# Performance work log

Measured on AMD Instinct MI355X. Metric: run time of the kernel, lower is better.

## Reference

```python
import jax, jax.numpy as jnp
import numpy as np

D_MAX = 0.5      # max_dist init kwarg
EPS_W = 1e-8     # weight for far edges
EPS_L = 1e-5     # diagonal jitter on projected Laplacian


def setup_inputs() -> dict:
    key = jax.random.key(0)
    k1, k2, k3, k4, k5 = jax.random.split(key, 5)
    V, d_feat, E, K = 8192, 128, 262144, 512
    # scale so squared distances straddle D_MAX (both branches taken)
    inputs = jax.random.normal(k1, (V, d_feat), dtype=jnp.float32) * 0.05
    src = jax.random.randint(k2, (E,), 0, V)
    off = jax.random.randint(k3, (E,), 1, V)  # avoid self-loops
    dst = (src + off) % V
    edge_index = jnp.stack([src, dst]).astype(jnp.int32)
    A = jax.random.normal(k4, (K, K), dtype=jnp.float32)
    targets = A @ A.T / K + jnp.eye(K, dtype=jnp.float32)  # SPD covariance
    pmat = jax.random.normal(k5, (K, V), dtype=jnp.float32) / np.float32(np.sqrt(V))
    return {"inputs": inputs, "targets": targets, "edge_index": edge_index, "pmat": pmat}


def reference(inputs, targets, edge_index, pmat):
    V = inputs.shape[0]
    K = pmat.shape[0]
    src, dst = edge_index[0], edge_index[1]
    # vectorized per-edge squared distance + thresholded weight
    d = jnp.sum((inputs[src] - inputs[dst]) ** 2, axis=-1)            # [E]
    w = jnp.where(d <= D_MAX, jnp.exp(-d), jnp.float32(EPS_W))        # [E]
    # W = I on diag, w on (i,j) and (j,i) for edges, 0 elsewhere
    W = jnp.eye(V, dtype=inputs.dtype).at[src, dst].set(w).at[dst, src].set(w)
    deg = W.sum(axis=1)                                               # [V]
    idx = jnp.arange(V)
    L = (-W).at[idx, idx].add(deg)                                    # Laplacian D - W
    L_adj = (pmat @ L) @ pmat.T + EPS_L * jnp.eye(K, dtype=inputs.dtype)
    # log det(inv(L_adj)) = -logdet(L_adj); trace(L_adj @ S0) = sum(L_adj * S0^T)
    logdet_Ladj = jnp.linalg.slogdet(L_adj)[1]
    logdet_S0 = jnp.linalg.slogdet(targets)[1]
    tr = jnp.sum(L_adj * targets.T)
    return -logdet_Ladj - logdet_S0 - jnp.float32(K) + tr
```

## Files before the change

### kernel.cpp

```cpp
#include <hip/hip_runtime.h>
#include <math.h>

#define V_N 8192
#define D_F 128
#define E_N 262144
#define K_N 512
#define DMAXF 0.5f
#define EPSW 1e-8f
#define EPSL 1e-5f
#define MAX_SE 16384
#define NZ_SYRK 24

#define NB_TR 4096
#define NB_ED (E_N / 16)
#define NB_CP 256

__global__ __launch_bounds__(256) void k_pre(const float* __restrict__ P, float* __restrict__ PT,
                                             const float* __restrict__ X, const int* __restrict__ ei,
                                             int* __restrict__ cnt, int* __restrict__ si,
                                             int* __restrict__ sj, float* __restrict__ sw,
                                             unsigned* __restrict__ htab,
                                             const float* __restrict__ T, float* __restrict__ Lw1) {
  __shared__ float tile[32][33];
  int b = blockIdx.x;
  if (b < NB_TR) {
    int v0 = (b & 255) * 32, k0 = (b >> 8) * 32;
    int tx = threadIdx.x & 31, ty = threadIdx.x >> 5;
#pragma unroll
    for (int i = 0; i < 4; ++i)
      tile[ty + i * 8][tx] = P[(size_t)(k0 + ty + i * 8) * V_N + v0 + tx];
    __syncthreads();
#pragma unroll
    for (int i = 0; i < 4; ++i)
      PT[(size_t)(v0 + ty + i * 8) * K_N + k0 + tx] = tile[tx][ty + i * 8];
  } else if (b < NB_TR + NB_ED) {
    int t = (b - NB_TR) * 256 + threadIdx.x;
    int e = t >> 4, lane = t & 15;
    int i = ei[e], j = ei[E_N + e];
    const float4* xi = (const float4*)(X + (size_t)i * D_F);
    const float4* xj = (const float4*)(X + (size_t)j * D_F);
    float4 a0 = xi[lane * 2], a1 = xi[lane * 2 + 1];
    float4 b0 = xj[lane * 2], b1 = xj[lane * 2 + 1];
    float d = 0.f, dx;
    dx = a0.x - b0.x; d += dx * dx;
    dx = a0.y - b0.y; d += dx * dx;
    dx = a0.z - b0.z; d += dx * dx;
    dx = a0.w - b0.w; d += dx * dx;
    dx = a1.x - b1.x; d += dx * dx;
    dx = a1.y - b1.y; d += dx * dx;
    dx = a1.z - b1.z; d += dx * dx;
    dx = a1.w - b1.w; d += dx * dx;
    d += __shfl_xor(d, 1);
    d += __shfl_xor(d, 2);
    d += __shfl_xor(d, 4);
    d += __shfl_xor(d, 8);
    if (lane == 0 && d <= DMAXF) {
      float w = expf(-d);
      unsigned a = (unsigned)min(i, j), bb = (unsigned)max(i, j);
      unsigned key = a * 8192u + bb;
      unsigned h = (key * 2654435761u) >> 16;
      bool isnew = false;
      for (int probe = 0; probe < 65536; ++probe) {
        unsigned slot = (h + (unsigned)probe) & 65535u;
        unsigned prev = atomicCAS(&htab[slot], 0u, key);
        if (prev == 0u) { isnew = true; break; }
        if (prev == key) break;
      }
      if (isnew) {
        int p = atomicAdd(cnt, 1);
        if (p < MAX_SE) { si[p] = i; sj[p] = j; sw[p] = w; }
      }
    }
  } else {
    int idx = (b - NB_TR - NB_ED) * 256 + threadIdx.x;
    ((float4*)Lw1)[idx] = ((const float4*)T)[idx];
  }
}

__global__ __launch_bounds__(256) void k_syrk(const int* __restrict__ cnt, const int* __restrict__ si,
                                              const int* __restrict__ sj, const float* __restrict__ sw,
                                              const float* __restrict__ PT, float* __restrict__ La,
                                              const float* __restrict__ T, float* __restrict__ tr) {
  int p = blockIdx.x, bj = 0;
  while (p >= 8 - bj) { p -= 8 - bj; ++bj; }
  int bi = bj + p;
  int r0g = bi * 64, c0g = bj * 64;
  int m = min(*cnt, MAX_SE);
  int chunk = (m + NZ_SYRK - 1) / NZ_SYRK;
  int e0 = blockIdx.y * chunk;
  int e1 = min(m, e0 + chunk);

  __shared__ float As[16][68];
  __shared__ float Bs[16][68];
  int tid = threadIdx.x;
  int le = tid >> 4, f = tid & 15;
  int r0 = (tid >> 4) * 4, c0 = (tid & 15) * 4;
  float acc[4][4];
#pragma unroll
  for (int i = 0; i < 4; ++i)
#pragma unroll
    for (int j = 0; j < 4; ++j) acc[i][j] = 0.f;

  float w_ = 0.f;
  float4 ai = make_float4(0.f, 0.f, 0.f, 0.f), aj = ai, ci = ai, cj = ai;
  {
    int e = e0 + le;
    if (e < e1) {
      int i = si[e], j = sj[e];
      w_ = sw[e];
      const float* pi = &PT[(size_t)i * K_N];
      const float* pj = &PT[(size_t)j * K_N];
      ai = *(const float4*)(pi + r0g + f * 4);
      aj = *(const float4*)(pj + r0g + f * 4);
      if (bi != bj) {
        ci = *(const float4*)(pi + c0g + f * 4);
        cj = *(const float4*)(pj + c0g + f * 4);
      }
    }
  }

  for (int es = e0; es < e1; es += 16) {
    float sq = sqrtf(w_);
    float4 qa, qb;
    qa.x = sq * (ai.x - aj.x); qa.y = sq * (ai.y - aj.y);
    qa.z = sq * (ai.z - aj.z); qa.w = sq * (ai.w - aj.w);
    if (bi != bj) {
      qb.x = sq * (ci.x - cj.x); qb.y = sq * (ci.y - cj.y);
      qb.z = sq * (ci.z - cj.z); qb.w = sq * (ci.w - cj.w);
    } else {
      qb = qa;
    }
    __syncthreads();
    *(float4*)&As[le][f * 4] = qa;
    *(float4*)&Bs[le][f * 4] = qb;
    __syncthreads();

    {
      int e = es + 16 + le;
      w_ = 0.f;
      if (e < e1) {
        int i = si[e], j = sj[e];
        w_ = sw[e];
        const float* pi = &PT[(size_t)i * K_N];
        const float* pj = &PT[(size_t)j * K_N];
        ai = *(const float4*)(pi + r0g + f * 4);
        aj = *(const float4*)(pj + r0g + f * 4);
        if (bi != bj) {
          ci = *(const float4*)(pi + c0g + f * 4);
          cj = *(const float4*)(pj + c0g + f * 4);
        }
      }
    }

#pragma unroll
    for (int k = 0; k < 16; ++k) {
      float4 av = *(const float4*)&As[k][r0];
      float4 bv = *(const float4*)&Bs[k][c0];
      acc[0][0] += av.x * bv.x; acc[0][1] += av.x * bv.y; acc[0][2] += av.x * bv.z; acc[0][3] += av.x * bv.w;
      acc[1][0] += av.y * bv.x; acc[1][1] += av.y * bv.y; acc[1][2] += av.y * bv.z; acc[1][3] += av.y * bv.w;
      acc[2][0] += av.z * bv.x; acc[2][1] += av.z * bv.y; acc[2][2] += av.z * bv.z; acc[2][3] += av.z * bv.w;
      acc[3][0] += av.w * bv.x; acc[3][1] += av.w * bv.y; acc[3][2] += av.w * bv.z; acc[3][3] += av.w * bv.w;
    }
  }

  bool addeps = (blockIdx.y == 0) && (bi == bj);
  float tdot = 0.f;
#pragma unroll
  for (int i = 0; i < 4; ++i)
#pragma unroll
    for (int j = 0; j < 4; ++j) {
      float v = acc[i][j];
      int rg = r0g + r0 + i, cg = c0g + c0 + j;
      if (addeps && rg == cg) v += EPSL;
      atomicAdd(&La[(size_t)rg * K_N + cg], v);
      float sc = (bi != bj) ? 2.f : (rg == cg ? 1.f : (rg > cg ? 2.f : 0.f));
      if (sc != 0.f) tdot += sc * v * T[(size_t)rg * K_N + cg];
    }
  tdot += __shfl_down(tdot, 32); tdot += __shfl_down(tdot, 16); tdot += __shfl_down(tdot, 8);
  tdot += __shfl_down(tdot, 4);  tdot += __shfl_down(tdot, 2);  tdot += __shfl_down(tdot, 1);
  if ((tid & 63) == 0) atomicAdd(tr, tdot);
}

__device__ __forceinline__ void factor32(float (*sm)[65], int o, int tid, float& logacc) {
  if (tid < 64) {
    int r = tid & 31;
    float a[32];
#pragma unroll
    for (int c = 0; c < 32; ++c) a[c] = sm[o + r][o + c];
    float ls = 0.f;
#pragma unroll
    for (int c = 0; c < 32; ++c) {
      float dc = __shfl(a[c], c);
      ls += logf(dc);
      float s_ = sqrtf(dc);
      a[c] = a[c] / s_;
#pragma unroll
      for (int k = c + 1; k < 32; ++k)
        a[k] -= a[c] * __shfl(a[c], k);
    }
    if (tid < 32) {
#pragma unroll
      for (int c = 0; c < 32; ++c) sm[o + r][o + c] = a[c];
    }
    if (tid == 0) logacc += ls;
  }
}

__global__ __launch_bounds__(512) void k_panel(float* La, float* Lw1, float* __restrict__ ld, int s) {
  float* A = (blockIdx.x == 0) ? La : Lw1;
  const int j0 = s * 64;
  int tid = threadIdx.x;
  __shared__ float sm[64][65];
  __shared__ float smT[64][68];
  __shared__ float rinv[64];
  float logacc = 0.f;

  for (int i = tid; i < 4096; i += 512) {
    int r = i >> 6, c = i & 63;
    sm[r][c] = A[(size_t)(j0 + r) * K_N + j0 + c];
  }
  __syncthreads();

  factor32(sm, 0, tid, logacc);
  __syncthreads();

  if (tid < 32) {
    int r = 32 + tid;
    float x[32];
#pragma unroll
    for (int c = 0; c < 32; ++c) x[c] = sm[r][c];
#pragma unroll
    for (int c = 0; c < 32; ++c) {
      x[c] = x[c] / sm[c][c];
#pragma unroll
      for (int k = c + 1; k < 32; ++k)
        x[k] -= x[c] * sm[k][c];
    }
#pragma unroll
    for (int c = 0; c < 32; ++c) sm[r][c] = x[c];
  }
  __syncthreads();

  for (int i = tid; i < 1024; i += 512) {
    int r = 32 + (i >> 5), c = 32 + (i & 31);
    float accv = 0.f;
#pragma unroll
    for (int k = 0; k < 32; ++k) accv += sm[r][k] * sm[c][k];
    sm[r][c] -= accv;
  }
  __syncthreads();

  factor32(sm, 32, tid, logacc);
  __syncthreads();

  for (int i = tid; i < 4096; i += 512) {
    int r = i >> 6, c = i & 63;
    smT[c][r] = sm[r][c];
  }
  if (tid < 64) rinv[tid] = 1.0f / sm[tid][tid];
  __syncthreads();

  int rrow = j0 + 64 + tid;
  if (rrow < K_N) {
    float x[64];
#pragma unroll
    for (int q = 0; q < 16; ++q) {
      float4 f = *(const float4*)&A[(size_t)rrow * K_N + j0 + 4 * q];
      x[4 * q] = f.x; x[4 * q + 1] = f.y; x[4 * q + 2] = f.z; x[4 * q + 3] = f.w;
    }
#pragma unroll
    for (int c = 0; c < 64; ++c) {
      x[c] *= rinv[c];
#pragma unroll
      for (int k = c + 1; k < 64; ++k)
        x[k] -= x[c] * smT[c][k];
    }
#pragma unroll
    for (int q = 0; q < 16; ++q) {
      float4 f;
      f.x = x[4 * q]; f.y = x[4 * q + 1]; f.z = x[4 * q + 2]; f.w = x[4 * q + 3];
      *(float4*)&A[(size_t)rrow * K_N + j0 + 4 * q] = f;
    }
  }

  for (int i = tid; i < 4096; i += 512) {
    int r = i >> 6, c = i & 63;
    A[(size_t)(j0 + r) * K_N + j0 + c] = sm[r][c];
  }
  if (tid == 0) ld[blockIdx.x * 8 + s] = logacc;
}

__global__ __launch_bounds__(256) void k_update(float* La, float* Lw1, int s) {
  float* A = (blockIdx.y == 0) ? La : Lw1;
  int nt = 7 - s;
  int p = blockIdx.x;
  int bj = 0;
  while (p >= nt - bj) { p -= nt - bj; ++bj; }
  int bi = bj + p;
  int r0g = (s + 1 + bi) * 64, c0g = (s + 1 + bj) * 64, k0g = s * 64;

  __shared__ float As[64][68];
  __shared__ float Bs[64][68];
  int tid = threadIdx.x;
  for (int i = tid; i < 1024; i += 256) {
    int r = i >> 4, kq = (i & 15) << 2;
    float4 f = *(const float4*)&A[(size_t)(r0g + r) * K_N + k0g + kq];
    As[kq + 0][r] = f.x; As[kq + 1][r] = f.y; As[kq + 2][r] = f.z; As[kq + 3][r] = f.w;
    float4 g = *(const float4*)&A[(size_t)(c0g + r) * K_N + k0g + kq];
    Bs[kq + 0][r] = g.x; Bs[kq + 1][r] = g.y; Bs[kq + 2][r] = g.z; Bs[kq + 3][r] = g.w;
  }
  __syncthreads();

  int r0 = (tid >> 4) * 4, c0 = (tid & 15) * 4;
  float acc[4][4];
#pragma unroll
  for (int i = 0; i < 4; ++i)
#pragma unroll
    for (int j = 0; j < 4; ++j) acc[i][j] = 0.f;
#pragma unroll 4
  for (int k = 0; k < 64; ++k) {
    float4 av = *(const float4*)&As[k][r0];
    float4 bv = *(const float4*)&Bs[k][c0];
    acc[0][0] += av.x * bv.x; acc[0][1] += av.x * bv.y; acc[0][2] += av.x * bv.z; acc[0][3] += av.x * bv.w;
    acc[1][0] += av.y * bv.x; acc[1][1] += av.y * bv.y; acc[1][2] += av.y * bv.z; acc[1][3] += av.y * bv.w;
    acc[2][0] += av.z * bv.x; acc[2][1] += av.z * bv.y; acc[2][2] += av.z * bv.z; acc[2][3] += av.z * bv.w;
    acc[3][0] += av.w * bv.x; acc[3][1] += av.w * bv.y; acc[3][2] += av.w * bv.z; acc[3][3] += av.w * bv.w;
  }
#pragma unroll
  for (int i = 0; i < 4; ++i) {
    float* cp = &A[(size_t)(r0g + r0 + i) * K_N + c0g + c0];
#pragma unroll
    for (int j = 0; j < 4; ++j) cp[j] = cp[j] - acc[i][j];
  }
}

__global__ void k_combine(const float* __restrict__ ld, const float* __restrict__ tr, float* __restrict__ out) {
  float l0 = 0.f, l1 = 0.f;
#pragma unroll
  for (int s = 0; s < 8; ++s) { l0 += ld[s]; l1 += ld[8 + s]; }
  out[0] = -l0 - l1 - (float)K_N + tr[0];
}

extern "C" void kernel_launch(void* const* d_in, const int* in_sizes, int n_in,
                              void* d_out, int out_size, void* d_ws, size_t ws_size,
                              hipStream_t stream) {
  const float* X  = (const float*)d_in[0];
  const float* T  = (const float*)d_in[1];
  const int*   ei = (const int*)d_in[2];
  const float* P  = (const float*)d_in[3];
  float* out = (float*)d_out;
  char* ws = (char*)d_ws;

  int*      cnt  = (int*)(ws + 0);
  float*    tr   = (float*)(ws + 16);
  float*    ld   = (float*)(ws + 32);
  unsigned* htab = (unsigned*)(ws + 4096);
  float*    La   = (float*)(ws + 266240);
  float*    Lw1  = (float*)(ws + 1314816);
  int*      si   = (int*)(ws + 2363392);
  int*      sj   = (int*)(ws + 2428928);
  float*    sw   = (float*)(ws + 2494464);
  float*    PT   = (float*)(ws + 2560000);

  hipMemsetAsync(ws, 0, 1314816, stream);

  k_pre<<<NB_TR + NB_ED + NB_CP, 256, 0, stream>>>(P, PT, X, ei, cnt, si, sj, sw, htab, T, Lw1);
  k_syrk<<<dim3(36, NZ_SYRK), 256, 0, stream>>>(cnt, si, sj, sw, PT, La, T, tr);

  for (int s = 0; s < 8; ++s) {
    k_panel<<<2, 512, 0, stream>>>(La, Lw1, ld, s);
    int nt = 7 - s;
    if (nt > 0) k_update<<<dim3(nt * (nt + 1) / 2, 2), 256, 0, stream>>>(La, Lw1, s);
  }
  k_combine<<<1, 1, 0, stream>>>(ld, tr, out);
}
```

Measured before the change: 553.0 us.

## Fuse blocked Cholesky into one persistent kernel with grid barriers; split pre-kernel

Replaces the 8-step loop of panel and update launches with a single persistent kernel of 16 blocks, 8 per matrix. The blocks sync through global atomic barriers and do a look-ahead, where the diagonal tile is updated into shared memory and factored as one 64-wide block instead of two 32-wide halves. The pre-kernel is split into a transpose/copy kernel that now uses 64x64 tiles with float4 access, and a separate edge kernel that uses 8 lanes per edge instead of 16. The aim is to cut about 15 launch gaps from the serial factorization. The cost is that it relies on all blocks being co-resident for the spin barrier, and the fixed small grid limits parallelism in the update phase.

```diff
diff --git a/kernel.cpp b/kernel.cpp
--- a/kernel.cpp
+++ b/kernel.cpp
@@ -10,70 +10,76 @@
 #define EPSL 1e-5f
 #define MAX_SE 16384
 #define NZ_SYRK 24
-
-#define NB_TR 4096
-#define NB_ED (E_N / 16)
-#define NB_CP 256
-
-__global__ __launch_bounds__(256) void k_pre(const float* __restrict__ P, float* __restrict__ PT,
-                                             const float* __restrict__ X, const int* __restrict__ ei,
-                                             int* __restrict__ cnt, int* __restrict__ si,
-                                             int* __restrict__ sj, float* __restrict__ sw,
-                                             unsigned* __restrict__ htab,
-                                             const float* __restrict__ T, float* __restrict__ Lw1) {
-  __shared__ float tile[32][33];
-  int b = blockIdx.x;
-  if (b < NB_TR) {
-    int v0 = (b & 255) * 32, k0 = (b >> 8) * 32;
-    int tx = threadIdx.x & 31, ty = threadIdx.x >> 5;
-#pragma unroll
-    for (int i = 0; i < 4; ++i)
-      tile[ty + i * 8][tx] = P[(size_t)(k0 + ty + i * 8) * V_N + v0 + tx];
+#define LDS68 68
+
+__global__ __launch_bounds__(256) void k_tr(const float* __restrict__ P, float* __restrict__ PT,
+                                            const float* __restrict__ T, float* __restrict__ Lw1) {
+  int b = blockIdx.x, tid = threadIdx.x;
+  if (b < 1024) {
+    __shared__ float tl[64][65];
+    int v0 = (b & 127) * 64, k0 = (b >> 7) * 64;
+    int c4 = tid & 15, rq = tid >> 4;
+#pragma unroll
+    for (int rr = 0; rr < 4; ++rr) {
+      int r = rq + 16 * rr;
+      float4 f = *(const float4*)&P[(size_t)(k0 + r) * V_N + v0 + c4 * 4];
+      tl[r][c4 * 4 + 0] = f.x; tl[r][c4 * 4 + 1] = f.y;
+      tl[r][c4 * 4 + 2] = f.z; tl[r][c4 * 4 + 3] = f.w;
+    }
     __syncthreads();
 #pragma unroll
-    for (int i = 0; i < 4; ++i)
-      PT[(size_t)(v0 + ty + i * 8) * K_N + k0 + tx] = tile[tx][ty + i * 8];
-  } else if (b < NB_TR + NB_ED) {
-    int t = (b - NB_TR) * 256 + threadIdx.x;
-    int e = t >> 4, lane = t & 15;
-    int i = ei[e], j = ei[E_N + e];
-    const float4* xi = (const float4*)(X + (size_t)i * D_F);
-    const float4* xj = (const float4*)(X + (size_t)j * D_F);
-    float4 a0 = xi[lane * 2], a1 = xi[lane * 2 + 1];
-    float4 b0 = xj[lane * 2], b1 = xj[lane * 2 + 1];
-    float d = 0.f, dx;
-    dx = a0.x - b0.x; d += dx * dx;
-    dx = a0.y - b0.y; d += dx * dx;
-    dx = a0.z - b0.z; d += dx * dx;
-    dx = a0.w - b0.w; d += dx * dx;
-    dx = a1.x - b1.x; d += dx * dx;
-    dx = a1.y - b1.y; d += dx * dx;
-    dx = a1.z - b1.z; d += dx * dx;
-    dx = a1.w - b1.w; d += dx * dx;
-    d += __shfl_xor(d, 1);
-    d += __shfl_xor(d, 2);
-    d += __shfl_xor(d, 4);
-    d += __shfl_xor(d, 8);
-    if (lane == 0 && d <= DMAXF) {
-      float w = expf(-d);
-      unsigned a = (unsigned)min(i, j), bb = (unsigned)max(i, j);
-      unsigned key = a * 8192u + bb;
-      unsigned h = (key * 2654435761u) >> 16;
-      bool isnew = false;
-      for (int probe = 0; probe < 65536; ++probe) {
-        unsigned slot = (h + (unsigned)probe) & 65535u;
-        unsigned prev = atomicCAS(&htab[slot], 0u, key);
-        if (prev == 0u) { isnew = true; break; }
-        if (prev == key) break;
-      }
-      if (isnew) {
-        int p = atomicAdd(cnt, 1);
-        if (p < MAX_SE) { si[p] = i; sj[p] = j; sw[p] = w; }
-      }
+    for (int rr = 0; rr < 4; ++rr) {
+      int r = rq + 16 * rr;
+      float4 f;
+      f.x = tl[c4 * 4 + 0][r]; f.y = tl[c4 * 4 + 1][r];
+      f.z = tl[c4 * 4 + 2][r]; f.w = tl[c4 * 4 + 3][r];
+      *(float4*)&PT[(size_t)(v0 + r) * K_N + k0 + c4 * 4] = f;
     }
   } else {
-    int idx = (b - NB_TR - NB_ED) * 256 + threadIdx.x;
+    int idx = (b - 1024) * 256 + tid;
     ((float4*)Lw1)[idx] = ((const float4*)T)[idx];
+  }
+}
+
+__global__ __launch_bounds__(256) void k_edge(const float* __restrict__ X, const int* __restrict__ ei,
+                                              int* __restrict__ cnt, int* __restrict__ si,
+                                              int* __restrict__ sj, float* __restrict__ sw,
+                                              unsigned* __restrict__ htab) {
+  int t = blockIdx.x * 256 + threadIdx.x;
+  int e = t >> 3, lane = t & 7;
+  int i = ei[e], j = ei[E_N + e];
+  const float4* xi = (const float4*)(X + (size_t)i * D_F);
+  const float4* xj = (const float4*)(X + (size_t)j * D_F);
+  float4 A0 = xi[lane * 4 + 0], A1 = xi[lane * 4 + 1], A2 = xi[lane * 4 + 2], A3 = xi[lane * 4 + 3];
+  float4 B0 = xj[lane * 4 + 0], B1 = xj[lane * 4 + 1], B2 = xj[lane * 4 + 2], B3 = xj[lane * 4 + 3];
+  float d = 0.f, dx;
+  dx = A0.x - B0.x; d += dx * dx; dx = A0.y - B0.y; d += dx * dx;
+  dx = A0.z - B0.z; d += dx * dx; dx = A0.w - B0.w; d += dx * dx;
+  dx = A1.x - B1.x; d += dx * dx; dx = A1.y - B1.y; d += dx * dx;
+  dx = A1.z - B1.z; d += dx * dx; dx = A1.w - B1.w; d += dx * dx;
+  dx = A2.x - B2.x; d += dx * dx; dx = A2.y - B2.y; d += dx * dx;
+  dx = A2.z - B2.z; d += dx * dx; dx = A2.w - B2.w; d += dx * dx;
+  dx = A3.x - B3.x; d += dx * dx; dx = A3.y - B3.y; d += dx * dx;
+  dx = A3.z - B3.z; d += dx * dx; dx = A3.w - B3.w; d += dx * dx;
+  d += __shfl_xor(d, 1);
+  d += __shfl_xor(d, 2);
+  d += __shfl_xor(d, 4);
+  if (lane == 0 && d <= DMAXF) {
+    float w = expf(-d);
+    unsigned a = (unsigned)min(i, j), bb = (unsigned)max(i, j);
+    unsigned key = a * 8192u + bb;
+    unsigned h = (key * 2654435761u) >> 16;
+    bool isnew = false;
+    for (int probe = 0; probe < 65536; ++probe) {
+      unsigned slot = (h + (unsigned)probe) & 65535u;
+      unsigned prev = atomicCAS(&htab[slot], 0u, key);
+      if (prev == 0u) { isnew = true; break; }
+      if (prev == key) break;
+    }
+    if (isnew) {
+      int p = atomicAdd(cnt, 1);
+      if (p < MAX_SE) { si[p] = i; sj[p] = j; sw[p] = w; }
+    }
   }
 }
 
@@ -181,156 +187,180 @@
   if ((tid & 63) == 0) atomicAdd(tr, tdot);
 }
 
-__device__ __forceinline__ void factor32(float (*sm)[65], int o, int tid, float& logacc) {
-  if (tid < 64) {
-    int r = tid & 31;
-    float a[32];
-#pragma unroll
-    for (int c = 0; c < 32; ++c) a[c] = sm[o + r][o + c];
-    float ls = 0.f;
-#pragma unroll
-    for (int c = 0; c < 32; ++c) {
-      float dc = __shfl(a[c], c);
-      ls += logf(dc);
-      float s_ = sqrtf(dc);
-      a[c] = a[c] / s_;
-#pragma unroll
-      for (int k = c + 1; k < 32; ++k)
-        a[k] -= a[c] * __shfl(a[c], k);
-    }
-    if (tid < 32) {
-#pragma unroll
-      for (int c = 0; c < 32; ++c) sm[o + r][o + c] = a[c];
-    }
-    if (tid == 0) logacc += ls;
-  }
-}
-
-__global__ __launch_bounds__(512) void k_panel(float* La, float* Lw1, float* __restrict__ ld, int s) {
-  float* A = (blockIdx.x == 0) ? La : Lw1;
-  const int j0 = s * 64;
-  int tid = threadIdx.x;
-  __shared__ float sm[64][65];
-  __shared__ float smT[64][68];
-  __shared__ float rinv[64];
-  float logacc = 0.f;
-
-  for (int i = tid; i < 4096; i += 512) {
-    int r = i >> 6, c = i & 63;
-    sm[r][c] = A[(size_t)(j0 + r) * K_N + j0 + c];
-  }
+__device__ __forceinline__ void gbar(unsigned* c_, unsigned& ep) {
+  ep += 8;
   __syncthreads();
-
-  factor32(sm, 0, tid, logacc);
+  __threadfence();
+  if (threadIdx.x == 0) {
+    __hip_atomic_fetch_add(c_, 1u, __ATOMIC_RELEASE, __HIP_MEMORY_SCOPE_AGENT);
+    while (__hip_atomic_load(c_, __ATOMIC_ACQUIRE, __HIP_MEMORY_SCOPE_AGENT) < ep)
+      __builtin_amdgcn_s_sleep(2);
+  }
   __syncthreads();
-
-  if (tid < 32) {
-    int r = 32 + tid;
-    float x[32];
-#pragma unroll
-    for (int c = 0; c < 32; ++c) x[c] = sm[r][c];
-#pragma unroll
-    for (int c = 0; c < 32; ++c) {
-      x[c] = x[c] / sm[c][c];
-#pragma unroll
-      for (int k = c + 1; k < 32; ++k)
-        x[k] -= x[c] * sm[k][c];
-    }
-#pragma unroll
-    for (int c = 0; c < 32; ++c) sm[r][c] = x[c];
-  }
+  __threadfence();
+}
+
+__device__ __forceinline__ void factor64(float* A, int j0, const float* smFsrc,
+                                         float* ldout, int tid) {
+  if (tid >= 64) return;
+  int r = tid;
+  float a[64];
+  if (smFsrc) {
+#pragma unroll
+    for (int q = 0; q < 16; ++q) {
+      float4 f = *(const float4*)&smFsrc[r * LDS68 + q * 4];
+      a[q * 4 + 0] = f.x; a[q * 4 + 1] = f.y; a[q * 4 + 2] = f.z; a[q * 4 + 3] = f.w;
+    }
+  } else {
+#pragma unroll
+    for (int q = 0; q < 16; ++q) {
+      float4 f = *(const float4*)&A[(size_t)(j0 + r) * K_N + j0 + q * 4];
+      a[q * 4 + 0] = f.x; a[q * 4 + 1] = f.y; a[q * 4 + 2] = f.z; a[q * 4 + 3] = f.w;
+    }
+  }
+  float ls = 0.f;
+#pragma unroll
+  for (int c = 0; c < 64; ++c) {
+    float dc = __shfl(a[c], c);
+    ls += logf(dc);
+    float rs = rsqrtf(dc);
+    a[c] *= rs;
+#pragma unroll
+    for (int k = c + 1; k < 64; ++k)
+      a[k] -= a[c] * __shfl(a[c], k);
+  }
+#pragma unroll
+  for (int q = 0; q < 16; ++q) {
+    float4 f;
+    f.x = a[q * 4 + 0]; f.y = a[q * 4 + 1]; f.z = a[q * 4 + 2]; f.w = a[q * 4 + 3];
+    *(float4*)&A[(size_t)(j0 + r) * K_N + j0 + q * 4] = f;
+  }
+  if (r == 0) *ldout = ls;
+}
+
+__device__ __forceinline__ void upd_tile(float* A, int sbase, int q, int nt2, bool toSmF,
+                                         float* As_, float* Bs_, float* smF, int tid) {
+  int lbj = 0;
+  while (q >= nt2 - lbj) { q -= nt2 - lbj; ++lbj; }
+  int lbi = lbj + q;
+  int r0g = (sbase + lbi) * 64, c0g = (sbase + lbj) * 64, k0g = (sbase - 1) * 64;
   __syncthreads();
-
   for (int i = tid; i < 1024; i += 512) {
-    int r = 32 + (i >> 5), c = 32 + (i & 31);
-    float accv = 0.f;
-#pragma unroll
-    for (int k = 0; k < 32; ++k) accv += sm[r][k] * sm[c][k];
-    sm[r][c] -= accv;
-  }
-  __syncthreads();
-
-  factor32(sm, 32, tid, logacc);
-  __syncthreads();
-
-  for (int i = tid; i < 4096; i += 512) {
-    int r = i >> 6, c = i & 63;
-    smT[c][r] = sm[r][c];
-  }
-  if (tid < 64) rinv[tid] = 1.0f / sm[tid][tid];
-  __syncthreads();
-
-  int rrow = j0 + 64 + tid;
-  if (rrow < K_N) {
-    float x[64];
-#pragma unroll
-    for (int q = 0; q < 16; ++q) {
-      float4 f = *(const float4*)&A[(size_t)rrow * K_N + j0 + 4 * q];
-      x[4 * q] = f.x; x[4 * q + 1] = f.y; x[4 * q + 2] = f.z; x[4 * q + 3] = f.w;
-    }
-#pragma unroll
-    for (int c = 0; c < 64; ++c) {
-      x[c] *= rinv[c];
-#pragma unroll
-      for (int k = c + 1; k < 64; ++k)
-        x[k] -= x[c] * smT[c][k];
-    }
-#pragma unroll
-    for (int q = 0; q < 16; ++q) {
-      float4 f;
-      f.x = x[4 * q]; f.y = x[4 * q + 1]; f.z = x[4 * q + 2]; f.w = x[4 * q + 3];
-      *(float4*)&A[(size_t)rrow * K_N + j0 + 4 * q] = f;
-    }
-  }
-
-  for (int i = tid; i < 4096; i += 512) {
-    int r = i >> 6, c = i & 63;
-    A[(size_t)(j0 + r) * K_N + j0 + c] = sm[r][c];
-  }
-  if (tid == 0) ld[blockIdx.x * 8 + s] = logacc;
-}
-
-__global__ __launch_bounds__(256) void k_update(float* La, float* Lw1, int s) {
-  float* A = (blockIdx.y == 0) ? La : Lw1;
-  int nt = 7 - s;
-  int p = blockIdx.x;
-  int bj = 0;
-  while (p >= nt - bj) { p -= nt - bj; ++bj; }
-  int bi = bj + p;
-  int r0g = (s + 1 + bi) * 64, c0g = (s + 1 + bj) * 64, k0g = s * 64;
-
-  __shared__ float As[64][68];
-  __shared__ float Bs[64][68];
-  int tid = threadIdx.x;
-  for (int i = tid; i < 1024; i += 256) {
     int r = i >> 4, kq = (i & 15) << 2;
     float4 f = *(const float4*)&A[(size_t)(r0g + r) * K_N + k0g + kq];
-    As[kq + 0][r] = f.x; As[kq + 1][r] = f.y; As[kq + 2][r] = f.z; As[kq + 3][r] = f.w;
+    As_[(kq + 0) * LDS68 + r] = f.x; As_[(kq + 1) * LDS68 + r] = f.y;
+    As_[(kq + 2) * LDS68 + r] = f.z; As_[(kq + 3) * LDS68 + r] = f.w;
     float4 g = *(const float4*)&A[(size_t)(c0g + r) * K_N + k0g + kq];
-    Bs[kq + 0][r] = g.x; Bs[kq + 1][r] = g.y; Bs[kq + 2][r] = g.z; Bs[kq + 3][r] = g.w;
+    Bs_[(kq + 0) * LDS68 + r] = g.x; Bs_[(kq + 1) * LDS68 + r] = g.y;
+    Bs_[(kq + 2) * LDS68 + r] = g.z; Bs_[(kq + 3) * LDS68 + r] = g.w;
   }
   __syncthreads();
-
-  int r0 = (tid >> 4) * 4, c0 = (tid & 15) * 4;
-  float acc[4][4];
-#pragma unroll
-  for (int i = 0; i < 4; ++i)
+  int r0 = (tid >> 4) * 2, c0 = (tid & 15) * 4;
+  float acc[2][4];
+#pragma unroll
+  for (int i = 0; i < 2; ++i)
 #pragma unroll
     for (int j = 0; j < 4; ++j) acc[i][j] = 0.f;
-#pragma unroll 4
+#pragma unroll 8
   for (int k = 0; k < 64; ++k) {
-    float4 av = *(const float4*)&As[k][r0];
-    float4 bv = *(const float4*)&Bs[k][c0];
-    acc[0][0] += av.x * bv.x; acc[0][1] += av.x * bv.y; acc[0][2] += av.x * bv.z; acc[0][3] += av.x * bv.w;
-    acc[1][0] += av.y * bv.x; acc[1][1] += av.y * bv.y; acc[1][2] += av.y * bv.z; acc[1][3] += av.y * bv.w;
-    acc[2][0] += av.z * bv.x; acc[2][1] += av.z * bv.y; acc[2][2] += av.z * bv.z; acc[2][3] += av.z * bv.w;
-    acc[3][0] += av.w * bv.x; acc[3][1] += av.w * bv.y; acc[3][2] += av.w * bv.z; acc[3][3] += av.w * bv.w;
-  }
-#pragma unroll
-  for (int i = 0; i < 4; ++i) {
-    float* cp = &A[(size_t)(r0g + r0 + i) * K_N + c0g + c0];
-#pragma unroll
-    for (int j = 0; j < 4; ++j) cp[j] = cp[j] - acc[i][j];
+    float a0 = As_[k * LDS68 + r0], a1 = As_[k * LDS68 + r0 + 1];
+    float4 bv = *(const float4*)&Bs_[k * LDS68 + c0];
+    acc[0][0] += a0 * bv.x; acc[0][1] += a0 * bv.y; acc[0][2] += a0 * bv.z; acc[0][3] += a0 * bv.w;
+    acc[1][0] += a1 * bv.x; acc[1][1] += a1 * bv.y; acc[1][2] += a1 * bv.z; acc[1][3] += a1 * bv.w;
+  }
+  if (toSmF) {
+#pragma unroll
+    for (int i = 0; i < 2; ++i) {
+      const float* cp = &A[(size_t)(r0g + r0 + i) * K_N + c0g + c0];
+      float4 co = *(const float4*)cp;
+      smF[(r0 + i) * LDS68 + c0 + 0] = co.x - acc[i][0];
+      smF[(r0 + i) * LDS68 + c0 + 1] = co.y - acc[i][1];
+      smF[(r0 + i) * LDS68 + c0 + 2] = co.z - acc[i][2];
+      smF[(r0 + i) * LDS68 + c0 + 3] = co.w - acc[i][3];
+    }
+  } else {
+#pragma unroll
+    for (int i = 0; i < 2; ++i) {
+      float* cp = &A[(size_t)(r0g + r0 + i) * K_N + c0g + c0];
+      cp[0] -= acc[i][0]; cp[1] -= acc[i][1]; cp[2] -= acc[i][2]; cp[3] -= acc[i][3];
+    }
+  }
+}
+
+__global__ __launch_bounds__(512, 1) void k_chol2(float* La, float* Lw1, float* __restrict__ ld,
+                                                  unsigned* __restrict__ ctr) {
+  int mat = blockIdx.x >> 3;
+  int b = blockIdx.x & 7;
+  float* A = mat ? Lw1 : La;
+  unsigned* myctr = ctr + mat * 16;
+  int tid = threadIdx.x;
+  __shared__ float sh[3 * 64 * LDS68 + 64];
+  float* As_ = sh;
+  float* Bs_ = sh + 64 * LDS68;
+  float* smF = sh + 2 * 64 * LDS68;
+  float* rin = sh + 3 * 64 * LDS68;
+  unsigned ep = 0;
+  __threadfence();
+
+  for (int s = 0; s < 8; ++s) {
+    const int j0 = s * 64;
+    int rel = (b - s) & 7;
+    if (s == 0) {
+      if (b == 0) factor64(A, 0, nullptr, &ld[mat * 8], tid);
+    } else {
+      int nt2 = 8 - s;
+      int cntT = nt2 * (nt2 + 1) / 2;
+      if (rel == 0) {
+        upd_tile(A, s, 0, nt2, true, As_, Bs_, smF, tid);
+        __syncthreads();
+        factor64(A, j0, smF, &ld[mat * 8 + s], tid);
+      } else {
+        for (int q = rel; q < cntT; q += 7)
+          upd_tile(A, s, q, nt2, false, As_, Bs_, smF, tid);
+      }
+    }
+    gbar(myctr, ep);
+
+    if (b < 7 - s) {
+      __syncthreads();
+      for (int idx = tid; idx < 4096; idx += 512) {
+        int k = idx >> 6, c = idx & 63;
+        As_[c * LDS68 + k] = A[(size_t)(j0 + k) * K_N + j0 + c];
+      }
+      __syncthreads();
+      if (tid < 64) rin[tid] = 1.0f / As_[tid * LDS68 + tid];
+      __syncthreads();
+      if (tid < 64) {
+        int row = (s + 1 + b) * 64 + tid;
+        float x[64];
+#pragma unroll
+        for (int q = 0; q < 16; ++q) {
+          float4 f = *(const float4*)&A[(size_t)row * K_N + j0 + q * 4];
+          x[q * 4 + 0] = f.x; x[q * 4 + 1] = f.y; x[q * 4 + 2] = f.z; x[q * 4 + 3] = f.w;
+        }
+#pragma unroll
+        for (int c = 0; c < 64; ++c) {
+          float xc = x[c] * rin[c];
+          x[c] = xc;
+          int kk = c + 1;
+#pragma unroll
+          for (; kk < 64 && (kk & 3); ++kk) x[kk] -= xc * As_[c * LDS68 + kk];
+#pragma unroll
+          for (; kk < 64; kk += 4) {
+            float4 f = *(const float4*)&As_[c * LDS68 + kk];
+            x[kk + 0] -= xc * f.x; x[kk + 1] -= xc * f.y;
+            x[kk + 2] -= xc * f.z; x[kk + 3] -= xc * f.w;
+          }
+        }
+#pragma unroll
+        for (int q = 0; q < 16; ++q) {
+          float4 f;
+          f.x = x[q * 4 + 0]; f.y = x[q * 4 + 1]; f.z = x[q * 4 + 2]; f.w = x[q * 4 + 3];
+          *(float4*)&A[(size_t)row * K_N + j0 + q * 4] = f;
+        }
+      }
+    }
+    gbar(myctr, ep);
   }
 }
 
@@ -354,6 +384,7 @@
   int*      cnt  = (int*)(ws + 0);
   float*    tr   = (float*)(ws + 16);
   float*    ld   = (float*)(ws + 32);
+  unsigned* bar  = (unsigned*)(ws + 128);
   unsigned* htab = (unsigned*)(ws + 4096);
   float*    La   = (float*)(ws + 266240);
   float*    Lw1  = (float*)(ws + 1314816);
@@ -364,13 +395,9 @@
 
   hipMemsetAsync(ws, 0, 1314816, stream);
 
-  k_pre<<<NB_TR + NB_ED + NB_CP, 256, 0, stream>>>(P, PT, X, ei, cnt, si, sj, sw, htab, T, Lw1);
+  k_tr<<<1280, 256, 0, stream>>>(P, PT, T, Lw1);
+  k_edge<<<E_N / 32, 256, 0, stream>>>(X, ei, cnt, si, sj, sw, htab);
   k_syrk<<<dim3(36, NZ_SYRK), 256, 0, stream>>>(cnt, si, sj, sw, PT, La, T, tr);
-
-  for (int s = 0; s < 8; ++s) {
-    k_panel<<<2, 512, 0, stream>>>(La, Lw1, ld, s);
-    int nt = 7 - s;
-    if (nt > 0) k_update<<<dim3(nt * (nt + 1) / 2, 2), 256, 0, stream>>>(La, Lw1, s);
-  }
+  k_chol2<<<16, 512, 0, stream>>>(La, Lw1, ld, bar);
   k_combine<<<1, 1, 0, stream>>>(ld, tr, out);
 }
```

Result: slower. 1.024 ms (+85.1%).
